# Optimization experiments

Hardware: AMD Instinct MI355X
Metric: run time of the kernel (lower is better)

## Reference

```python
import jax, jax.numpy as jnp
import numpy as np

N, F_IN, HID, E1, E2, P = 100000, 128, 128, 800000, 800000, 200000


def setup_inputs() -> dict:
    key = jax.random.key(0)
    ks = jax.random.split(key, 9)
    x = jax.random.normal(ks[0], (N, F_IN), dtype=jnp.float32)
    edge_index1 = jax.random.randint(ks[1], (2, E1), 0, N)
    edge_index2 = jax.random.randint(ks[2], (2, E2), 0, N)
    edge_weight1 = jax.random.uniform(ks[3], (E1,), dtype=jnp.float32)
    edge_weight2 = jax.random.uniform(ks[4], (E2,), dtype=jnp.float32)
    pos_edge_index = jax.random.randint(ks[5], (2, P), 0, N)
    # parameters (fan-in scaled init)
    W1 = jax.random.normal(ks[6], (F_IN, HID), dtype=jnp.float32) / np.sqrt(F_IN)
    W2 = jax.random.normal(ks[7], (HID, HID), dtype=jnp.float32) / np.sqrt(HID)
    Wlin = jax.random.normal(ks[8], (2, 2 * HID), dtype=jnp.float32) / np.sqrt(2 * HID)  # torch Linear [out,in]
    return {"x": x, "edge_index1": edge_index1, "edge_index2": edge_index2,
            "edge_weight1": edge_weight1, "edge_weight2": edge_weight2,
            "pos_edge_index": pos_edge_index, "W1": W1, "W2": W2, "Wlin": Wlin}


def gcn_conv(x, W, edge_index, edge_weight, num_nodes):
    # GCNConv(add_self_loops=False, normalize=False, bias=False):
    # out[i] = sum_{(j->i) in E} w_e * (x @ W)[j]
    xw = x @ W                                    # [N, H]
    msg = xw[edge_index[0]] * edge_weight[:, None]  # [E, H] gather + scale
    return jax.ops.segment_sum(msg, edge_index[1], num_segments=num_nodes)


def reference(x, edge_index1, edge_index2, edge_weight1, edge_weight2,
              pos_edge_index, W1, W2, Wlin):
    n = x.shape[0]
    h = jax.nn.relu(gcn_conv(x, W1, edge_index1, edge_weight1, n))
    z = gcn_conv(h, W2, edge_index2, edge_weight2, n)          # [N, H]
    pair = jnp.concatenate([z[pos_edge_index[0]], z[pos_edge_index[1]]], axis=1)  # [P, 2H]
    return pair @ Wlin.T                                        # [P, 2]
```

## Files before the change

kernel.cpp:

```cpp
#include <hip/hip_runtime.h>

#define F 128
#define BSH 9
#define BSZ 512
#define NBLKA 256
#define MAXBIN 256
#define CSTRIDE 16

typedef __bf16 bf16x8 __attribute__((ext_vector_type(8)));
typedef unsigned short ushort8 __attribute__((ext_vector_type(8)));
typedef float f32x4 __attribute__((ext_vector_type(4)));

static __device__ __forceinline__ unsigned short f2bf(float f) {
    unsigned int u = __float_as_uint(f);
    u += 0x7fffu + ((u >> 16) & 1u);
    return (unsigned short)(u >> 16);
}
static __device__ __forceinline__ void bf2x(unsigned int u, float& lo, float& hi) {
    lo = __uint_as_float(u << 16);
    hi = __uint_as_float(u & 0xffff0000u);
}

#define WPITCH 136

template <int RELU, int INBF>
__global__ __launch_bounds__(256) void gemm128_mfma(const void* __restrict__ Xv,
                                                    const float* __restrict__ W,
                                                    unsigned short* __restrict__ Y,
                                                    int n,
                                                    int* __restrict__ z1,
                                                    int* __restrict__ z2, int zn) {
    if (zn > 0) {
        if (blockIdx.x == 0) { for (int i = threadIdx.x; i < zn; i += 256) z1[i] = 0; }
        else if (blockIdx.x == 1) { for (int i = threadIdx.x; i < zn; i += 256) z2[i] = 0; }
    }
    __shared__ __align__(16) unsigned short WT[F * WPITCH];
    for (int idx = threadIdx.x; idx < F * F; idx += 256) {
        const int k = idx >> 7, c = idx & 127;
        WT[c * WPITCH + k] = f2bf(W[idx]);
    }
    __syncthreads();

    const int lane = threadIdx.x & 63;
    const int wv = threadIdx.x >> 6;
    const int m15 = lane & 15;
    const int quad = lane >> 4;
    const int rowBase = blockIdx.x * 128 + wv * 32;

    f32x4 acc[2][8];
#pragma unroll
    for (int rt = 0; rt < 2; ++rt)
#pragma unroll
        for (int ct = 0; ct < 8; ++ct) acc[rt][ct] = (f32x4){0.f, 0.f, 0.f, 0.f};

    int rA[2];
    rA[0] = min(rowBase + m15, n - 1);
    rA[1] = min(rowBase + 16 + m15, n - 1);

#pragma unroll
    for (int ks = 0; ks < 4; ++ks) {
        const int k0 = ks * 32 + quad * 8;
        bf16x8 a[2];
#pragma unroll
        for (int rt = 0; rt < 2; ++rt) {
            if (INBF) {
                const unsigned short* Xb = (const unsigned short*)Xv;
                ushort8 u = *(const ushort8*)(Xb + (size_t)rA[rt] * F + k0);
                if (RELU) {
#pragma unroll
                    for (int j = 0; j < 8; ++j) u[j] = (u[j] & 0x8000u) ? 0 : u[j];
                }
                a[rt] = __builtin_bit_cast(bf16x8, u);
            } else {
                const float* Xf = (const float*)Xv;
                const float* p = Xf + (size_t)rA[rt] * F + k0;
                float4 lo = *(const float4*)p;
                float4 hi = *(const float4*)(p + 4);
                if (RELU) {
                    lo.x = fmaxf(lo.x, 0.f); lo.y = fmaxf(lo.y, 0.f);
                    lo.z = fmaxf(lo.z, 0.f); lo.w = fmaxf(lo.w, 0.f);
                    hi.x = fmaxf(hi.x, 0.f); hi.y = fmaxf(hi.y, 0.f);
                    hi.z = fmaxf(hi.z, 0.f); hi.w = fmaxf(hi.w, 0.f);
                }
                ushort8 u;
                u[0] = f2bf(lo.x); u[1] = f2bf(lo.y); u[2] = f2bf(lo.z); u[3] = f2bf(lo.w);
                u[4] = f2bf(hi.x); u[5] = f2bf(hi.y); u[6] = f2bf(hi.z); u[7] = f2bf(hi.w);
                a[rt] = __builtin_bit_cast(bf16x8, u);
            }
        }
#pragma unroll
        for (int ct = 0; ct < 8; ++ct) {
            const int nn = ct * 16 + m15;
            const bf16x8 b = *(const bf16x8*)(WT + nn * WPITCH + k0);
            acc[0][ct] = __builtin_amdgcn_mfma_f32_16x16x32_bf16(a[0], b, acc[0][ct], 0, 0, 0);
            acc[1][ct] = __builtin_amdgcn_mfma_f32_16x16x32_bf16(a[1], b, acc[1][ct], 0, 0, 0);
        }
    }

#pragma unroll
    for (int rt = 0; rt < 2; ++rt)
#pragma unroll
        for (int reg = 0; reg < 4; ++reg) {
            const int row = rowBase + rt * 16 + quad * 4 + reg;
            if (row < n) {
#pragma unroll
                for (int ct = 0; ct < 8; ++ct)
                    Y[(size_t)row * F + ct * 16 + m15] = f2bf(acc[rt][ct][reg]);
            }
        }
}

__global__ __launch_bounds__(256) void scatter_both(
    const int* __restrict__ ei1, const float* __restrict__ ew1,
    const int* __restrict__ ei2, const float* __restrict__ ew2,
    int* __restrict__ bc1, int* __restrict__ bc2,
    uint2* __restrict__ Ep1, uint2* __restrict__ Ep2,
    int E1, int E2, int nbin, int cap) {
    __shared__ int h[MAXBIN], base[MAXBIN], cur[MAXBIN];
    const int layer2 = blockIdx.x >= NBLKA;
    const int blk = layer2 ? blockIdx.x - NBLKA : blockIdx.x;
    const int* __restrict__ ei = layer2 ? ei2 : ei1;
    const float* __restrict__ ew = layer2 ? ew2 : ew1;
    int* __restrict__ bc = layer2 ? bc2 : bc1;
    uint2* __restrict__ Ep = layer2 ? Ep2 : Ep1;
    const int E = layer2 ? E2 : E1;

    for (int i = threadIdx.x; i < nbin; i += 256) h[i] = 0;
    __syncthreads();
    const int chunk = (E + NBLKA - 1) / NBLKA;
    const int lo = blk * chunk;
    const int hi = min(lo + chunk, E);
    for (int e = lo + threadIdx.x; e < hi; e += 256)
        atomicAdd(&h[((unsigned)ei[E + e]) >> BSH], 1);
    __syncthreads();
    for (int i = threadIdx.x; i < nbin; i += 256) {
        cur[i] = 0;
        base[i] = h[i] ? atomicAdd(&bc[i * CSTRIDE], h[i]) : 0;
    }
    __syncthreads();
    for (int e = lo + threadIdx.x; e < hi; e += 256) {
        const unsigned int dst = (unsigned int)ei[E + e];
        const unsigned int src = (unsigned int)ei[e];
        const int b = (int)(dst >> BSH);
        const int slot = base[b] + atomicAdd(&cur[b], 1);
        if (slot < cap)
            Ep[(size_t)b * cap + slot] =
                make_uint2(src | ((dst & (BSZ - 1)) << 20), (unsigned)__float_as_int(ew[e]));
    }
}

__global__ __launch_bounds__(512) void sort_both(
    const uint2* __restrict__ Ep1, const uint2* __restrict__ Ep2,
    const int* __restrict__ bc1, const int* __restrict__ bc2,
    uint2* __restrict__ Sg1, uint2* __restrict__ Sg2,
    int2* __restrict__ eb1, int2* __restrict__ eb2,
    int n, int nbin, int cap) {
    __shared__ int hist[BSZ], pref[BSZ], cur[BSZ];
    const int layer2 = blockIdx.x >= nbin;
    const int bin = layer2 ? blockIdx.x - nbin : blockIdx.x;
    const uint2* __restrict__ Ep = layer2 ? Ep2 : Ep1;
    const int* __restrict__ bc = layer2 ? bc2 : bc1;
    uint2* __restrict__ Sg = layer2 ? Sg2 : Sg1;
    int2* __restrict__ eb = layer2 ? eb2 : eb1;
    const int tid = threadIdx.x;
    const int base = bin * cap;
    const int cnt = min(bc[bin * CSTRIDE], cap);
    hist[tid] = 0;
    __syncthreads();
    for (int i = tid; i < cnt; i += 512)
        atomicAdd(&hist[Ep[(size_t)base + i].x >> 20], 1);
    __syncthreads();
    pref[tid] = hist[tid];
    __syncthreads();
    for (int off = 1; off < BSZ; off <<= 1) {
        int t = (tid >= off) ? pref[tid - off] : 0;
        __syncthreads();
        pref[tid] += t;
        __syncthreads();
    }
    {
        const int inc = pref[tid];
        const int ex = inc - hist[tid];
        cur[tid] = ex;
        const int v = (bin << BSH) + tid;
        if (v < n) eb[v] = make_int2(base + ex, base + inc);
    }
    __syncthreads();
    for (int i = tid; i < cnt; i += 512) {
        const uint2 e = Ep[(size_t)base + i];
        const int pos = atomicAdd(&cur[e.x >> 20], 1);
        Sg[(size_t)base + pos] = make_uint2(e.x & 0xFFFFFu, e.y);
    }
}

template <int FUSE_U>
__global__ __launch_bounds__(256) void gather_agg(const unsigned short* __restrict__ XW,
                                                  const int2* __restrict__ ebounds,
                                                  const uint2* __restrict__ Sedge,
                                                  const float* __restrict__ Wlin,
                                                  unsigned short* __restrict__ OUT,
                                                  float4* __restrict__ U, int n) {
    __shared__ float WL[512];
    if (FUSE_U) {
        for (int i = threadIdx.x; i < 512; i += 256) WL[i] = Wlin[i];
        __syncthreads();
    }
    const int l = threadIdx.x & 15;
    const int v = blockIdx.x * 16 + (threadIdx.x >> 4);
    if (v >= n) return;
    float acc[8];
#pragma unroll
    for (int j = 0; j < 8; ++j) acc[j] = 0.f;
    const int2 be = ebounds[v];
    const int e2 = be.y;
    for (int p = be.x; p < e2; p += 4) {
        const int p1 = min(p + 1, e2 - 1);
        const int p2 = min(p + 2, e2 - 1);
        const int p3 = min(p + 3, e2 - 1);
        const uint2 s0 = Sedge[p],  s1 = Sedge[p1];
        const uint2 s2 = Sedge[p2], s3 = Sedge[p3];
        const uint4 x0 = ((const uint4*)(XW + (size_t)s0.x * F))[l];
        const uint4 x1 = ((const uint4*)(XW + (size_t)s1.x * F))[l];
        const uint4 x2 = ((const uint4*)(XW + (size_t)s2.x * F))[l];
        const uint4 x3 = ((const uint4*)(XW + (size_t)s3.x * F))[l];
        const float w0 = __int_as_float(s0.y);
        const float w1 = (p + 1 < e2) ? __int_as_float(s1.y) : 0.f;
        const float w2 = (p + 2 < e2) ? __int_as_float(s2.y) : 0.f;
        const float w3 = (p + 3 < e2) ? __int_as_float(s3.y) : 0.f;
        float a0, a1, a2, a3, a4, a5, a6, a7;
        bf2x(x0.x, a0, a1); bf2x(x0.y, a2, a3); bf2x(x0.z, a4, a5); bf2x(x0.w, a6, a7);
        acc[0] = fmaf(w0, a0, acc[0]); acc[1] = fmaf(w0, a1, acc[1]);
        acc[2] = fmaf(w0, a2, acc[2]); acc[3] = fmaf(w0, a3, acc[3]);
        acc[4] = fmaf(w0, a4, acc[4]); acc[5] = fmaf(w0, a5, acc[5]);
        acc[6] = fmaf(w0, a6, acc[6]); acc[7] = fmaf(w0, a7, acc[7]);
        bf2x(x1.x, a0, a1); bf2x(x1.y, a2, a3); bf2x(x1.z, a4, a5); bf2x(x1.w, a6, a7);
        acc[0] = fmaf(w1, a0, acc[0]); acc[1] = fmaf(w1, a1, acc[1]);
        acc[2] = fmaf(w1, a2, acc[2]); acc[3] = fmaf(w1, a3, acc[3]);
        acc[4] = fmaf(w1, a4, acc[4]); acc[5] = fmaf(w1, a5, acc[5]);
        acc[6] = fmaf(w1, a6, acc[6]); acc[7] = fmaf(w1, a7, acc[7]);
        bf2x(x2.x, a0, a1); bf2x(x2.y, a2, a3); bf2x(x2.z, a4, a5); bf2x(x2.w, a6, a7);
        acc[0] = fmaf(w2, a0, acc[0]); acc[1] = fmaf(w2, a1, acc[1]);
        acc[2] = fmaf(w2, a2, acc[2]); acc[3] = fmaf(w2, a3, acc[3]);
        acc[4] = fmaf(w2, a4, acc[4]); acc[5] = fmaf(w2, a5, acc[5]);
        acc[6] = fmaf(w2, a6, acc[6]); acc[7] = fmaf(w2, a7, acc[7]);
        bf2x(x3.x, a0, a1); bf2x(x3.y, a2, a3); bf2x(x3.z, a4, a5); bf2x(x3.w, a6, a7);
        acc[0] = fmaf(w3, a0, acc[0]); acc[1] = fmaf(w3, a1, acc[1]);
        acc[2] = fmaf(w3, a2, acc[2]); acc[3] = fmaf(w3, a3, acc[3]);
        acc[4] = fmaf(w3, a4, acc[4]); acc[5] = fmaf(w3, a5, acc[5]);
        acc[6] = fmaf(w3, a6, acc[6]); acc[7] = fmaf(w3, a7, acc[7]);
    }
    if (!FUSE_U) {
        ushort8 o;
#pragma unroll
        for (int j = 0; j < 8; ++j) o[j] = f2bf(acc[j]);
        *(ushort8*)(OUT + (size_t)v * F + (size_t)l * 8) = o;
    } else {
        const int k = l * 8;
        float s0 = 0.f, s1 = 0.f, s2 = 0.f, s3 = 0.f;
#pragma unroll
        for (int j = 0; j < 8; ++j) {
            s0 = fmaf(acc[j], WL[k + j],       s0);
            s1 = fmaf(acc[j], WL[128 + k + j], s1);
            s2 = fmaf(acc[j], WL[256 + k + j], s2);
            s3 = fmaf(acc[j], WL[384 + k + j], s3);
        }
#pragma unroll
        for (int off = 8; off > 0; off >>= 1) {
            s0 += __shfl_down(s0, off, 16);
            s1 += __shfl_down(s1, off, 16);
            s2 += __shfl_down(s2, off, 16);
            s3 += __shfl_down(s3, off, 16);
        }
        if (l == 0) U[v] = make_float4(s0, s1, s2, s3);
    }
}

__global__ __launch_bounds__(256) void pair_combine(const float4* __restrict__ U,
                                                    const int* __restrict__ pos,
                                                    float* __restrict__ out, int P) {
    const int p = blockIdx.x * 256 + threadIdx.x;
    if (p >= P) return;
    const int a = pos[p];
    const int b = pos[P + p];
    const float4 ua = U[a];
    const float4 ub = U[b];
    *(float2*)(out + (size_t)p * 2) = make_float2(ua.x + ub.y, ua.z + ub.w);
}

extern "C" void kernel_launch(void* const* d_in, const int* in_sizes, int n_in,
                              void* d_out, int out_size, void* d_ws, size_t ws_size,
                              hipStream_t stream) {
    const float* x    = (const float*)d_in[0];
    const int*   ei1  = (const int*)  d_in[1];
    const int*   ei2  = (const int*)  d_in[2];
    const float* ew1  = (const float*)d_in[3];
    const float* ew2  = (const float*)d_in[4];
    const int*   pos  = (const int*)  d_in[5];
    const float* W1   = (const float*)d_in[6];
    const float* W2   = (const float*)d_in[7];
    const float* Wlin = (const float*)d_in[8];
    float* out = (float*)d_out;

    const int N  = in_sizes[0] / F;
    const int E1 = in_sizes[1] / 2;
    const int E2 = in_sizes[2] / 2;
    const int P  = in_sizes[5] / 2;
    const int Emax = E1 > E2 ? E1 : E2;
    const int NBIN = (N + BSZ - 1) >> BSH;
    const int cap  = Emax / NBIN + 512;

    unsigned short* Abf = (unsigned short*)d_ws;
    unsigned short* Bbf = Abf + (size_t)N * F;
    uintptr_t up  = (uintptr_t)(Bbf + (size_t)N * F);
    up = (up + 15) & ~(uintptr_t)15;
    float4* U     = (float4*)up;
    int2*   eb1   = (int2*)(U + N);
    int2*   eb2   = eb1 + N;
    int*    bc1   = (int*)(eb2 + N);
    int*    bc2   = bc1 + NBIN * CSTRIDE;
    uintptr_t sp  = (uintptr_t)(bc2 + NBIN * CSTRIDE);
    sp = (sp + 15) & ~(uintptr_t)15;
    uint2* Ep1   = (uint2*)sp;
    uint2* Sg1   = Ep1 + (size_t)NBIN * cap;
    uint2* Ep2   = Sg1 + (size_t)NBIN * cap;
    uint2* Sg2   = Ep2 + (size_t)NBIN * cap;

    gemm128_mfma<0, 0><<<(N + 127) / 128, 256, 0, stream>>>(
        x, W1, Abf, N, bc1, bc2, NBIN * CSTRIDE);
    scatter_both<<<2 * NBLKA, 256, 0, stream>>>(
        ei1, ew1, ei2, ew2, bc1, bc2, Ep1, Ep2, E1, E2, NBIN, cap);
    sort_both<<<2 * NBIN, 512, 0, stream>>>(
        Ep1, Ep2, bc1, bc2, Sg1, Sg2, eb1, eb2, N, NBIN, cap);
    gather_agg<0><<<(N + 15) / 16, 256, 0, stream>>>(Abf, eb1, Sg1, Wlin, Bbf, U, N);
    gemm128_mfma<1, 1><<<(N + 127) / 128, 256, 0, stream>>>(
        Bbf, W2, Abf, N, nullptr, nullptr, 0);
    gather_agg<1><<<(N + 15) / 16, 256, 0, stream>>>(Abf, eb2, Sg2, Wlin, Bbf, U, N);
    pair_combine<<<(P + 255) / 256, 256, 0, stream>>>(U, pos, out, P);
}
```

Baseline: 254.2 us.

## Fuse layer-1 GEMM with edge scatter and stage GEMM output through LDS

Merges the first dense GEMM and the edge-binning scatter into one launch, with block ranges split between the two jobs, so both independent stages can share the GPU at once. Bin counter zeroing moves to a hipMemsetAsync, since the scatter now runs concurrently with the GEMM that used to do it. GEMM outputs are staged in shared memory and written back as 16-byte row-contiguous stores instead of scattered 2-byte stores. Costs are an extra memset call, extra LDS barriers in the GEMM epilogue, and a fused kernel whose LDS footprint is sized for the GEMM even in scatter blocks.

```diff
diff --git a/kernel.cpp b/kernel.cpp
--- a/kernel.cpp
+++ b/kernel.cpp
@@ -22,19 +22,14 @@
 }
 
 #define WPITCH 136
+#define CPITCH 136
+#define LDSN (F * WPITCH)
 
 template <int RELU, int INBF>
-__global__ __launch_bounds__(256) void gemm128_mfma(const void* __restrict__ Xv,
-                                                    const float* __restrict__ W,
-                                                    unsigned short* __restrict__ Y,
-                                                    int n,
-                                                    int* __restrict__ z1,
-                                                    int* __restrict__ z2, int zn) {
-    if (zn > 0) {
-        if (blockIdx.x == 0) { for (int i = threadIdx.x; i < zn; i += 256) z1[i] = 0; }
-        else if (blockIdx.x == 1) { for (int i = threadIdx.x; i < zn; i += 256) z2[i] = 0; }
-    }
-    __shared__ __align__(16) unsigned short WT[F * WPITCH];
+static __device__ void gemm_body(const void* __restrict__ Xv,
+                                 const float* __restrict__ W,
+                                 unsigned short* __restrict__ Y,
+                                 int n, int blk, unsigned short* __restrict__ WT) {
     for (int idx = threadIdx.x; idx < F * F; idx += 256) {
         const int k = idx >> 7, c = idx & 127;
         WT[c * WPITCH + k] = f2bf(W[idx]);
@@ -45,7 +40,7 @@
     const int wv = threadIdx.x >> 6;
     const int m15 = lane & 15;
     const int quad = lane >> 4;
-    const int rowBase = blockIdx.x * 128 + wv * 32;
+    const int rowBase = blk * 128 + wv * 32;
 
     f32x4 acc[2][8];
 #pragma unroll
@@ -97,34 +92,34 @@
         }
     }
 
+    __syncthreads();
+    unsigned short* CW = WT + wv * 32 * CPITCH;
 #pragma unroll
     for (int rt = 0; rt < 2; ++rt)
 #pragma unroll
         for (int reg = 0; reg < 4; ++reg) {
-            const int row = rowBase + rt * 16 + quad * 4 + reg;
-            if (row < n) {
-#pragma unroll
-                for (int ct = 0; ct < 8; ++ct)
-                    Y[(size_t)row * F + ct * 16 + m15] = f2bf(acc[rt][ct][reg]);
-            }
-        }
-}
-
-__global__ __launch_bounds__(256) void scatter_both(
-    const int* __restrict__ ei1, const float* __restrict__ ew1,
-    const int* __restrict__ ei2, const float* __restrict__ ew2,
-    int* __restrict__ bc1, int* __restrict__ bc2,
-    uint2* __restrict__ Ep1, uint2* __restrict__ Ep2,
-    int E1, int E2, int nbin, int cap) {
-    __shared__ int h[MAXBIN], base[MAXBIN], cur[MAXBIN];
-    const int layer2 = blockIdx.x >= NBLKA;
-    const int blk = layer2 ? blockIdx.x - NBLKA : blockIdx.x;
-    const int* __restrict__ ei = layer2 ? ei2 : ei1;
-    const float* __restrict__ ew = layer2 ? ew2 : ew1;
-    int* __restrict__ bc = layer2 ? bc2 : bc1;
-    uint2* __restrict__ Ep = layer2 ? Ep2 : Ep1;
-    const int E = layer2 ? E2 : E1;
-
+            const int row = rt * 16 + quad * 4 + reg;
+#pragma unroll
+            for (int ct = 0; ct < 8; ++ct)
+                CW[row * CPITCH + ct * 16 + m15] = f2bf(acc[rt][ct][reg]);
+        }
+    __syncthreads();
+#pragma unroll
+    for (int j = 0; j < 8; ++j) {
+        const int row = j * 4 + quad;
+        const int grow = rowBase + row;
+        if (grow < n) {
+            ushort8 o = *(const ushort8*)(CW + row * CPITCH + m15 * 8);
+            *(ushort8*)(Y + (size_t)grow * F + m15 * 8) = o;
+        }
+    }
+}
+
+static __device__ void scatter_body(
+    const int* __restrict__ ei, const float* __restrict__ ew,
+    int* __restrict__ bc, uint2* __restrict__ Ep,
+    int E, int nbin, int cap, int blk, int* __restrict__ sh) {
+    int* h = sh; int* base = sh + MAXBIN; int* cur = sh + 2 * MAXBIN;
     for (int i = threadIdx.x; i < nbin; i += 256) h[i] = 0;
     __syncthreads();
     const int chunk = (E + NBLKA - 1) / NBLKA;
@@ -147,6 +142,34 @@
             Ep[(size_t)b * cap + slot] =
                 make_uint2(src | ((dst & (BSZ - 1)) << 20), (unsigned)__float_as_int(ew[e]));
     }
+}
+
+__global__ __launch_bounds__(256) void fused_gemm1_scatter(
+    const float* __restrict__ x, const float* __restrict__ W1,
+    unsigned short* __restrict__ Abf, int n,
+    const int* __restrict__ ei1, const float* __restrict__ ew1,
+    const int* __restrict__ ei2, const float* __restrict__ ew2,
+    int* __restrict__ bc1, int* __restrict__ bc2,
+    uint2* __restrict__ Ep1, uint2* __restrict__ Ep2,
+    int E1, int E2, int nbin, int cap) {
+    __shared__ __align__(16) unsigned short SH[LDSN];
+    if (blockIdx.x < 2 * NBLKA) {
+        const int layer2 = blockIdx.x >= NBLKA;
+        scatter_body(layer2 ? ei2 : ei1, layer2 ? ew2 : ew1,
+                     layer2 ? bc2 : bc1, layer2 ? Ep2 : Ep1,
+                     layer2 ? E2 : E1, nbin, cap,
+                     layer2 ? blockIdx.x - NBLKA : blockIdx.x, (int*)SH);
+    } else {
+        gemm_body<0, 0>(x, W1, Abf, n, blockIdx.x - 2 * NBLKA, SH);
+    }
+}
+
+__global__ __launch_bounds__(256) void gemm128_mfma_l2(const unsigned short* __restrict__ X,
+                                                       const float* __restrict__ W,
+                                                       unsigned short* __restrict__ Y,
+                                                       int n) {
+    __shared__ __align__(16) unsigned short WT[LDSN];
+    gemm_body<1, 1>(X, W, Y, n, blockIdx.x, WT);
 }
 
 __global__ __launch_bounds__(512) void sort_both(
@@ -325,15 +348,15 @@
     uint2* Ep2   = Sg1 + (size_t)NBIN * cap;
     uint2* Sg2   = Ep2 + (size_t)NBIN * cap;
 
-    gemm128_mfma<0, 0><<<(N + 127) / 128, 256, 0, stream>>>(
-        x, W1, Abf, N, bc1, bc2, NBIN * CSTRIDE);
-    scatter_both<<<2 * NBLKA, 256, 0, stream>>>(
-        ei1, ew1, ei2, ew2, bc1, bc2, Ep1, Ep2, E1, E2, NBIN, cap);
+    const int gB = (N + 127) / 128;
+
+    hipMemsetAsync(bc1, 0, (size_t)2 * NBIN * CSTRIDE * sizeof(int), stream);
+    fused_gemm1_scatter<<<2 * NBLKA + gB, 256, 0, stream>>>(
+        x, W1, Abf, N, ei1, ew1, ei2, ew2, bc1, bc2, Ep1, Ep2, E1, E2, NBIN, cap);
     sort_both<<<2 * NBIN, 512, 0, stream>>>(
         Ep1, Ep2, bc1, bc2, Sg1, Sg2, eb1, eb2, N, NBIN, cap);
     gather_agg<0><<<(N + 15) / 16, 256, 0, stream>>>(Abf, eb1, Sg1, Wlin, Bbf, U, N);
-    gemm128_mfma<1, 1><<<(N + 127) / 128, 256, 0, stream>>>(
-        Bbf, W2, Abf, N, nullptr, nullptr, 0);
+    gemm128_mfma_l2<<<gB, 256, 0, stream>>>(Bbf, W2, Abf, N);
     gather_agg<1><<<(N + 15) / 16, 256, 0, stream>>>(Abf, eb2, Sg2, Wlin, Bbf, U, N);
     pair_combine<<<(P + 255) / 256, 256, 0, stream>>>(U, pos, out, P);
 }
```

Result: faster. 245.4 us (-3.4%).
